# Kernel optimization log

Measured on AMD Instinct MI355X. Metric: run time of the kernel, lower is better.

The kernel has to match this reference:

```python
import jax, jax.numpy as jnp
import numpy as np

B = 8192      # batch size
D = 512       # feature dim == num_classes (centers is [C, C] in the original)
C = 512       # num_classes
MARGIN = 1.0


def setup_inputs() -> dict:
    key = jax.random.key(0)
    k1, k2, k3 = jax.random.split(key, 3)
    inputs = jax.random.normal(k1, (B, D), dtype=jnp.float32)
    targets = jax.random.randint(k2, (B,), 0, C)
    centers = jax.random.normal(k3, (C, D), dtype=jnp.float32)  # learned param
    return {"inputs": inputs, "targets": targets, "centers": centers}


def reference(inputs, targets, centers):
    # centers_batch[j] = centers[targets[j]]  (gather rows)
    cb = centers[targets]                                   # [B, D]
    # dist[i, j] = || inputs[i] - cb[j] ||_2, computed via the expanded form
    # (||a||^2 + ||b||^2 - 2 a.b) so we never materialize a [B, B, D] tensor.
    sq = ((inputs * inputs).sum(-1)[:, None]
          + (cb * cb).sum(-1)[None, :]
          - 2.0 * (inputs @ cb.T))                          # [B, B]
    dist = jnp.sqrt(jnp.clip(sq, 1e-12))                    # clamp(min=1e-12).sqrt()

    # mask[i, j] = (targets[i] == targets[j]); note original indexes dist[i][mask[i]]
    mask = targets[:, None] == targets[None, :]             # [B, B] bool
    dist_ap = jnp.max(jnp.where(mask, dist, -jnp.inf), axis=1)   # hardest positive per row
    dist_an = jnp.min(jnp.where(mask, jnp.inf, dist), axis=1)    # hardest negative per row

    # MarginRankingLoss(margin)(dist_an, dist_ap, y=1) = mean(relu(dist_ap - dist_an + margin))
    loss = jnp.mean(jnp.maximum(0.0, dist_ap - dist_an + MARGIN))
    prec = jnp.mean((dist_an > dist_ap).astype(jnp.float32))
    return loss, prec
```

## Files before the change

kernel.cpp:

```cpp
#include <hip/hip_runtime.h>
#include <hip/hip_bf16.h>

#define NB 8192
#define ND 512
#define NC 512
#define MARGIN_F 1.0f
#define BIGF 3.0e38f

typedef __attribute__((ext_vector_type(8))) short bf16x8;
typedef __attribute__((ext_vector_type(4))) float f32x4;

__device__ __forceinline__ unsigned fkey(float f) {
    unsigned u = __float_as_uint(f);
    unsigned mask = (u & 0x80000000u) ? 0xFFFFFFFFu : 0x80000000u;
    return u ^ mask;
}
__device__ __forceinline__ float finv(unsigned k) {
    unsigned mask = (k & 0x80000000u) ? 0x80000000u : 0xFFFFFFFFu;
    return __uint_as_float(k ^ mask);
}
__device__ __forceinline__ unsigned short f2bf(float f) {
    __hip_bfloat16 h = __float2bfloat16(f);
    return __builtin_bit_cast(unsigned short, h);
}

#define GLOAD_LDS16(g, l)                                                    \
    __builtin_amdgcn_global_load_lds(                                        \
        (const __attribute__((address_space(1))) void*)(g),                  \
        (__attribute__((address_space(3))) void*)(l), 16, 0, 0)

__global__ __launch_bounds__(256) void k0_prep(
    const float* __restrict__ inputs, const int* __restrict__ targets,
    const float* __restrict__ centers,
    unsigned short* __restrict__ inB, unsigned short* __restrict__ cenB,
    float* __restrict__ rsq, float* __restrict__ csq,
    unsigned* __restrict__ counts, unsigned* __restrict__ negmin)
{
    const int bid = blockIdx.x;
    const int tid = threadIdx.x;

    if (bid == 2176) {
        __shared__ unsigned hist[NC];
        for (int i = tid; i < NC; i += 256) hist[i] = 0u;
        __syncthreads();
        for (int i = tid; i < NB; i += 256) atomicAdd(&hist[targets[i]], 1u);
        __syncthreads();
        for (int i = tid; i < NC; i += 256) counts[i] = hist[i];
        return;
    }

    const int wave = tid >> 6, lane = tid & 63;
    const float* src;
    unsigned short* dst;
    float* sqdst;
    int row;
    bool is_input = (bid < 2048);
    if (is_input) {
        row   = bid * 4 + wave;
        src   = inputs + (size_t)row * ND;
        dst   = inB + (size_t)row * ND;
        sqdst = rsq + row;
    } else {
        row   = (bid - 2048) * 4 + wave;
        src   = centers + (size_t)row * ND;
        dst   = cenB + (size_t)row * ND;
        sqdst = csq + row;
    }

    float4 v1 = ((const float4*)src)[lane];
    float4 v2 = ((const float4*)src)[lane + 64];
    float s = v1.x*v1.x + v1.y*v1.y + v1.z*v1.z + v1.w*v1.w
            + v2.x*v2.x + v2.y*v2.y + v2.z*v2.z + v2.w*v2.w;

    ushort4 o1, o2;
    o1.x = f2bf(v1.x); o1.y = f2bf(v1.y); o1.z = f2bf(v1.z); o1.w = f2bf(v1.w);
    o2.x = f2bf(v2.x); o2.y = f2bf(v2.y); o2.z = f2bf(v2.z); o2.w = f2bf(v2.w);
    ((ushort4*)dst)[lane]      = o1;
    ((ushort4*)dst)[lane + 64] = o2;

    #pragma unroll
    for (int off = 32; off > 0; off >>= 1) s += __shfl_down(s, off);
    if (lane == 0) {
        *sqdst = s;
        if (is_input) negmin[row] = 0xFFFFFFFFu;
    }
}

__global__ __launch_bounds__(256) void k2_mfma(
    const unsigned short* __restrict__ Ain, const unsigned short* __restrict__ cenB,
    const int* __restrict__ targets, const unsigned* __restrict__ counts,
    const float* __restrict__ csq,
    unsigned* __restrict__ negmin, float* __restrict__ apval)
{
    __shared__ __align__(16) unsigned short As[128 * 32];
    __shared__ __align__(16) unsigned short Bs[64 * 32];
    __shared__ int      tgtL[128];
    __shared__ float    csqL[64];
    __shared__ unsigned ldsmin[128];

    const int tid  = threadIdx.x;
    const int w    = tid >> 6;
    const int lane = tid & 63;
    const int wm   = w >> 1;
    const int wn   = w & 1;
    const int qd   = lane >> 4;
    const int ln   = lane & 15;

    const int bid   = blockIdx.x;
    const int rbase = (bid & 63) * 128;
    const int cbase = (bid >> 6) * 64;

    if (tid < 128) { tgtL[tid] = targets[rbase + tid]; ldsmin[tid] = 0xFFFFFFFFu; }
    if (tid < 64) {
        const int c = cbase + tid;
        csqL[tid] = (counts[c] > 0u) ? csq[c] : BIGF;
    }

    const int arow0 = w * 32 + (lane >> 2);
    const int brow  = w * 16 + (lane >> 2);
    const int scol  = (lane & 3) * 8;
    const unsigned short* gA0 = Ain  + (size_t)(rbase + arow0)      * ND + scol;
    const unsigned short* gA1 = Ain  + (size_t)(rbase + arow0 + 16) * ND + scol;
    const unsigned short* gB  = cenB + (size_t)(cbase + brow)       * ND + scol;
    unsigned short* lA0 = &As[(w * 32)      * 32];
    unsigned short* lA1 = &As[(w * 32 + 16) * 32];
    unsigned short* lB  = &Bs[(w * 16)      * 32];

    f32x4 acc[4][2] = {};

    for (int kb = 0; kb < ND; kb += 32) {
        __syncthreads();
        GLOAD_LDS16(gA0 + kb, lA0);
        GLOAD_LDS16(gA1 + kb, lA1);
        GLOAD_LDS16(gB  + kb, lB);
        __syncthreads();

        bf16x8 a[4], b[2];
        #pragma unroll
        for (int i = 0; i < 4; ++i)
            a[i] = *(const bf16x8*)&As[(wm * 64 + i * 16 + ln) * 32 + qd * 8];
        #pragma unroll
        for (int j = 0; j < 2; ++j)
            b[j] = *(const bf16x8*)&Bs[(wn * 32 + j * 16 + ln) * 32 + qd * 8];
        #pragma unroll
        for (int i = 0; i < 4; ++i)
            #pragma unroll
            for (int j = 0; j < 2; ++j)
                acc[i][j] = __builtin_amdgcn_mfma_f32_16x16x32_bf16(a[i], b[j], acc[i][j], 0, 0, 0);
    }

    #pragma unroll
    for (int i = 0; i < 4; ++i) {
        #pragma unroll
        for (int r = 0; r < 4; ++r) {
            const int rlocal = wm * 64 + i * 16 + qd * 4 + r;
            const int grow   = rbase + rlocal;
            const int tr     = tgtL[rlocal];
            float m = BIGF;
            #pragma unroll
            for (int j = 0; j < 2; ++j) {
                const int clocal = wn * 32 + j * 16 + ln;
                const float val = csqL[clocal] - 2.0f * acc[i][j][r];
                if (cbase + clocal == tr) {
                    apval[grow] = val;
                } else {
                    m = fminf(m, val);
                }
            }
            #pragma unroll
            for (int off = 1; off < 16; off <<= 1)
                m = fminf(m, __shfl_xor(m, off));
            if (ln == 0) atomicMin(&ldsmin[rlocal], fkey(m));
        }
    }
    __syncthreads();
    if (tid < 128) {
        unsigned v = ldsmin[tid];
        if (v != 0xFFFFFFFFu) atomicMin(&negmin[rbase + tid], v);
    }
}

__global__ __launch_bounds__(1024) void k3_final(
    const float* __restrict__ rsq, const unsigned* __restrict__ negmin,
    const float* __restrict__ apval, float* __restrict__ out)
{
    __shared__ float sl[1024];
    __shared__ float sp[1024];
    const int tid = threadIdx.x;
    float a = 0.0f, p = 0.0f;
    for (int r = tid; r < NB; r += 1024) {
        float s  = rsq[r];
        float an = sqrtf(fmaxf(s + finv(negmin[r]), 1e-12f));
        float ap = sqrtf(fmaxf(s + apval[r], 1e-12f));
        a += fmaxf(0.0f, ap - an + MARGIN_F);
        p += (an > ap) ? 1.0f : 0.0f;
    }
    sl[tid] = a; sp[tid] = p;
    __syncthreads();
    #pragma unroll
    for (int s = 512; s > 0; s >>= 1) {
        if (tid < s) { sl[tid] += sl[tid + s]; sp[tid] += sp[tid + s]; }
        __syncthreads();
    }
    if (tid == 0) {
        out[0] = sl[0] / (float)NB;
        out[1] = sp[0] / (float)NB;
    }
}

extern "C" void kernel_launch(void* const* d_in, const int* in_sizes, int n_in,
                              void* d_out, int out_size, void* d_ws, size_t ws_size,
                              hipStream_t stream) {
    const float* inputs  = (const float*)d_in[0];
    const int*   targets = (const int*)d_in[1];
    const float* centers = (const float*)d_in[2];
    float* out = (float*)d_out;

    char* wp = (char*)d_ws;
    unsigned short* inB    = (unsigned short*)(wp);
    unsigned short* cenB   = (unsigned short*)(wp + 8388608);
    float*          rsq    = (float*)(wp + 8912896);
    float*          csqv   = (float*)(wp + 8945664);
    unsigned*       counts = (unsigned*)(wp + 8947712);
    unsigned*       negmin = (unsigned*)(wp + 8949760);
    float*          apval  = (float*)(wp + 8982528);

    k0_prep<<<2177, 256, 0, stream>>>(inputs, targets, centers,
                                      inB, cenB, rsq, csqv, counts, negmin);
    k2_mfma<<<512, 256, 0, stream>>>(inB, cenB, targets, counts, csqv,
                                     negmin, apval);
    k3_final<<<1, 1024, 0, stream>>>(rsq, negmin, apval, out);
}
```

Measured before the change: 94.35 us.

## Use fragment-ordered LDS layout and 64-wide K steps in MFMA kernel

Shared-memory tiles for A and B are now stored in MFMA fragment order: each 16x32 chunk sits contiguously, and each lane reads its bf16x8 at lane*8. This is meant to remove the LDS bank conflicts of the strided row reads. The K loop now advances 64 per iteration with two MFMA sub-steps, which halves the number of barrier pairs. The cost is more global-to-LDS loads per thread per step, with 16-byte loads that are less coalesced per row.

```diff
diff --git a/kernel.cpp b/kernel.cpp
--- a/kernel.cpp
+++ b/kernel.cpp
@@ -92,8 +92,8 @@
     const float* __restrict__ csq,
     unsigned* __restrict__ negmin, float* __restrict__ apval)
 {
-    __shared__ __align__(16) unsigned short As[128 * 32];
-    __shared__ __align__(16) unsigned short Bs[64 * 32];
+    __shared__ __align__(16) unsigned short As[16 * 512];
+    __shared__ __align__(16) unsigned short Bs[8 * 512];
     __shared__ int      tgtL[128];
     __shared__ float    csqL[64];
     __shared__ unsigned ldsmin[128];
@@ -103,8 +103,8 @@
     const int lane = tid & 63;
     const int wm   = w >> 1;
     const int wn   = w & 1;
-    const int qd   = lane >> 4;
     const int ln   = lane & 15;
+    const int kc8  = (lane >> 4) * 8;
 
     const int bid   = blockIdx.x;
     const int rbase = (bid & 63) * 128;
@@ -116,39 +116,52 @@
         csqL[tid] = (counts[c] > 0u) ? csq[c] : BIGF;
     }
 
-    const int arow0 = w * 32 + (lane >> 2);
-    const int brow  = w * 16 + (lane >> 2);
-    const int scol  = (lane & 3) * 8;
-    const unsigned short* gA0 = Ain  + (size_t)(rbase + arow0)      * ND + scol;
-    const unsigned short* gA1 = Ain  + (size_t)(rbase + arow0 + 16) * ND + scol;
-    const unsigned short* gB  = cenB + (size_t)(cbase + brow)       * ND + scol;
-    unsigned short* lA0 = &As[(w * 32)      * 32];
-    unsigned short* lA1 = &As[(w * 32 + 16) * 32];
-    unsigned short* lB  = &Bs[(w * 16)      * 32];
+    const unsigned short* gAp[4];
+    unsigned short*       lAp[4];
+    #pragma unroll
+    for (int t = 0; t < 4; ++t) {
+        const int cid = 4 * w + t;
+        const int rg = cid >> 1, kh = cid & 1;
+        gAp[t] = Ain + (size_t)(rbase + rg * 16 + ln) * ND + kh * 32 + kc8;
+        lAp[t] = &As[cid * 512];
+    }
+    const unsigned short* gBp[2];
+    unsigned short*       lBp[2];
+    #pragma unroll
+    for (int t = 0; t < 2; ++t) {
+        const int cid = 2 * w + t;
+        gBp[t] = cenB + (size_t)(cbase + w * 16 + ln) * ND + t * 32 + kc8;
+        lBp[t] = &Bs[cid * 512];
+    }
 
     f32x4 acc[4][2] = {};
 
-    for (int kb = 0; kb < ND; kb += 32) {
-        __syncthreads();
-        GLOAD_LDS16(gA0 + kb, lA0);
-        GLOAD_LDS16(gA1 + kb, lA1);
-        GLOAD_LDS16(gB  + kb, lB);
-        __syncthreads();
-
-        bf16x8 a[4], b[2];
-        #pragma unroll
-        for (int i = 0; i < 4; ++i)
-            a[i] = *(const bf16x8*)&As[(wm * 64 + i * 16 + ln) * 32 + qd * 8];
-        #pragma unroll
-        for (int j = 0; j < 2; ++j)
-            b[j] = *(const bf16x8*)&Bs[(wn * 32 + j * 16 + ln) * 32 + qd * 8];
-        #pragma unroll
-        for (int i = 0; i < 4; ++i)
+    for (int kb = 0; kb < ND; kb += 64) {
+        __syncthreads();
+        #pragma unroll
+        for (int t = 0; t < 4; ++t) GLOAD_LDS16(gAp[t] + kb, lAp[t]);
+        #pragma unroll
+        for (int t = 0; t < 2; ++t) GLOAD_LDS16(gBp[t] + kb, lBp[t]);
+        __syncthreads();
+
+        #pragma unroll
+        for (int ks = 0; ks < 2; ++ks) {
+            bf16x8 a[4], b[2];
+            #pragma unroll
+            for (int i = 0; i < 4; ++i)
+                a[i] = *(const bf16x8*)&As[((wm * 4 + i) * 2 + ks) * 512 + lane * 8];
             #pragma unroll
             for (int j = 0; j < 2; ++j)
-                acc[i][j] = __builtin_amdgcn_mfma_f32_16x16x32_bf16(a[i], b[j], acc[i][j], 0, 0, 0);
-    }
-
+                b[j] = *(const bf16x8*)&Bs[((wn * 2 + j) * 2 + ks) * 512 + lane * 8];
+            #pragma unroll
+            for (int i = 0; i < 4; ++i)
+                #pragma unroll
+                for (int j = 0; j < 2; ++j)
+                    acc[i][j] = __builtin_amdgcn_mfma_f32_16x16x32_bf16(a[i], b[j], acc[i][j], 0, 0, 0);
+        }
+    }
+
+    const int qd = lane >> 4;
     #pragma unroll
     for (int i = 0; i < 4; ++i) {
         #pragma unroll
```

Result: slower. 97.63 us (+3.5%).
